# Kernel optimization log

Measured on AMD Instinct MI355X. Metric: run time of the kernel, lower is better.

The kernel has to match this reference:

```python
import jax, jax.numpy as jnp
import numpy as np

N_NODES = 50000
NEG_SLOPE = 0.2  # PyG GATConv default LeakyReLU slope


def gat_conv(x, src, dst, W, att_src, att_dst, bias, heads, out_ch, concat):
    """PyG-style GATConv (dropout=0, add_self_loops omitted to match raw edge list usage).
    x: [N, in], W: [in, heads*out_ch], att_*: [1, heads, out_ch], bias: [heads*out_ch] or [out_ch].
    Messages flow src -> dst; softmax normalizes over incoming edges of each dst node."""
    N = x.shape[0]
    h = (x @ W).reshape(N, heads, out_ch)                      # [N,H,C]
    a_s = (h * att_src).sum(-1)                                # [N,H]
    a_d = (h * att_dst).sum(-1)                                # [N,H]
    e = jax.nn.leaky_relu(a_s[src] + a_d[dst], NEG_SLOPE)      # [E,H] per-edge logits
    m = jax.ops.segment_max(e, dst, num_segments=N)            # [N,H] stable softmax max
    p = jnp.exp(e - m[dst])                                    # [E,H]
    s = jax.ops.segment_sum(p, dst, num_segments=N)            # [N,H]
    alpha = p / (s[dst] + 1e-16)                               # [E,H] attention coeffs
    out = jax.ops.segment_sum(h[src] * alpha[:, :, None], dst, num_segments=N)  # [N,H,C]
    out = out.reshape(N, heads * out_ch) if concat else out.mean(axis=1)
    return out + bias


def setup_inputs() -> dict:
    key = jax.random.key(0)
    ks = jax.random.split(key, 10)
    in_ch, hid, heads, out_ch = 128, 32, 4, 64
    E = 800000
    x = jax.random.normal(ks[0], (N_NODES, in_ch), dtype=jnp.float32)
    edge_index = jax.random.randint(ks[1], (2, E), 0, N_NODES, dtype=jnp.int64)
    sc = 0.1
    return {
        "x": x,
        "edge_index": edge_index,
        "W1": jax.random.normal(ks[2], (in_ch, heads * hid), dtype=jnp.float32) * sc,
        "att_src1": jax.random.normal(ks[3], (1, heads, hid), dtype=jnp.float32) * sc,
        "att_dst1": jax.random.normal(ks[4], (1, heads, hid), dtype=jnp.float32) * sc,
        "b1": jnp.zeros((heads * hid,), dtype=jnp.float32),
        "W2": jax.random.normal(ks[5], (heads * hid, out_ch), dtype=jnp.float32) * sc,
        "att_src2": jax.random.normal(ks[6], (1, 1, out_ch), dtype=jnp.float32) * sc,
        "att_dst2": jax.random.normal(ks[7], (1, 1, out_ch), dtype=jnp.float32) * sc,
        "b2": jnp.zeros((out_ch,), dtype=jnp.float32),
    }


def reference(x, edge_index, W1, att_src1, att_dst1, b1, W2, att_src2, att_dst2, b2):
    src, dst = edge_index[0], edge_index[1]
    h = gat_conv(x, src, dst, W1, att_src1, att_dst1, b1, heads=4, out_ch=32, concat=True)
    h = jax.nn.elu(h)
    out = gat_conv(h, src, dst, W2, att_src2, att_dst2, b2, heads=1, out_ch=64, concat=False)
    return out
```

## Files before the change

kernel.cpp:

```cpp
#include <hip/hip_runtime.h>

#define N_NODES 50000
#define N_EDGES 800000
#define GEMM_BLKS ((N_NODES + 63) / 64)
#define FILL_BLKS 4096
#define RANGE 6250
#define EDGES_PER_BLK 1564
#define MAXDEG 64
#define AGG_BLKS (N_NODES / 4)
#define W1P_ITEMS (144 * 136)
#define W2P_ITEMS (80 * 136)

typedef __attribute__((ext_vector_type(8))) short bf16x8;
typedef __attribute__((ext_vector_type(4))) float f32x4;
typedef unsigned short u16;
typedef unsigned int u32;

__device__ __forceinline__ float lrelu(float x) { return x > 0.f ? x : 0.2f * x; }

__device__ __forceinline__ u16 f2bf(float f) {
    u32 u = __float_as_uint(f);
    return (u16)((u + 0x7FFFu + ((u >> 16) & 1u)) >> 16);
}
__device__ __forceinline__ float bflo(u32 w) { return __uint_as_float(w << 16); }
__device__ __forceinline__ float bfhi(u32 w) { return __uint_as_float(w & 0xFFFF0000u); }
__device__ __forceinline__ float elu(float x) { return x > 0.f ? x : __expf(x) - 1.f; }

__global__ __launch_bounds__(256) void k_prep(
    const float* __restrict__ W1, const float* __restrict__ as1v, const float* __restrict__ ad1v,
    const float* __restrict__ W2, const float* __restrict__ as2v, const float* __restrict__ ad2v,
    u16* __restrict__ Wt1p, u16* __restrict__ Wt2p, int* __restrict__ deg)
{
    int gid = blockIdx.x * 256 + threadIdx.x;
    for (int i = gid; i < N_NODES; i += 120 * 256) deg[i] = 0;
    if (gid < W1P_ITEMS) {
        int n = gid / 136, k = gid % 136;
        float v = 0.f;
        if (k < 128) {
            if (n < 128) v = W1[k * 128 + n];
            else if (n < 136) {
                int h = n - 128;
                const float* att = (h < 4) ? as1v : ad1v;
                int hh = h & 3;
                float s = 0.f;
                for (int c = 0; c < 32; ++c) s += W1[k * 128 + hh * 32 + c] * att[hh * 32 + c];
                v = s;
            }
        }
        Wt1p[gid] = f2bf(v);
    } else {
        int g2 = gid - W1P_ITEMS;
        if (g2 < W2P_ITEMS) {
            int n = g2 / 136, k = g2 % 136;
            float v = 0.f;
            if (k < 128) {
                if (n < 64) v = W2[k * 64 + n];
                else if (n == 64) { float s = 0.f; for (int c = 0; c < 64; ++c) s += W2[k * 64 + c] * as2v[c]; v = s; }
                else if (n == 65) { float s = 0.f; for (int c = 0; c < 64; ++c) s += W2[k * 64 + c] * ad2v[c]; v = s; }
            }
            Wt2p[g2] = f2bf(v);
        }
    }
}

__global__ __launch_bounds__(256) void k_fill(
    const int* __restrict__ src, const int* __restrict__ dst,
    int* __restrict__ deg, u16* __restrict__ col16)
{
    const int g = blockIdx.x & 7;
    const int b = blockIdx.x >> 3;
    const int lo = g * RANGE;
    const int hi = min(lo + RANGE, N_NODES);
    const int e0 = b * EDGES_PER_BLK;
    const int e1 = min(e0 + EDGES_PER_BLK, N_EDGES);
    for (int e = e0 + threadIdx.x; e < e1; e += 256) {
        int v = dst[e];
        if (v >= lo && v < hi) {
            int pos = atomicAdd(&deg[v], 1);
            if (pos < MAXDEG) col16[v * MAXDEG + pos] = (u16)src[e];
        }
    }
}

__global__ __launch_bounds__(256, 4) void k_gemm1(
    const float* __restrict__ x, const u16* __restrict__ Wt1p,
    u16* __restrict__ hbf, float* __restrict__ as_, float* __restrict__ ad_)
{
    __shared__ u16 ws[144][136];
    const int t = threadIdx.x;
    const int n0 = blockIdx.x * 64;
    const int l = t & 63, w = t >> 6;
    const int lm = l & 15, quad = l >> 4;
    #pragma unroll
    for (int it = 0; it < 10; ++it) {
        int idx = it * 256 + t;
        if (idx < 2448) ((uint4*)&ws[0][0])[idx] = ((const uint4*)Wt1p)[idx];
    }
    const int nrow = n0 + w * 16 + lm;
    bf16x8 af[4];
    if (nrow < N_NODES) {
        const float* xr = &x[(size_t)nrow * 128];
        #pragma unroll
        for (int kc = 0; kc < 4; ++kc) {
            int k0 = kc * 32 + quad * 8;
            float4 v0 = *(const float4*)&xr[k0];
            float4 v1 = *(const float4*)&xr[k0 + 4];
            bf16x8 a;
            a[0] = (short)f2bf(v0.x); a[1] = (short)f2bf(v0.y);
            a[2] = (short)f2bf(v0.z); a[3] = (short)f2bf(v0.w);
            a[4] = (short)f2bf(v1.x); a[5] = (short)f2bf(v1.y);
            a[6] = (short)f2bf(v1.z); a[7] = (short)f2bf(v1.w);
            af[kc] = a;
        }
    } else {
        #pragma unroll
        for (int kc = 0; kc < 4; ++kc) af[kc] = (bf16x8){0, 0, 0, 0, 0, 0, 0, 0};
    }
    __syncthreads();
    f32x4 acc[9];
    #pragma unroll
    for (int nt = 0; nt < 9; ++nt) acc[nt] = (f32x4){0.f, 0.f, 0.f, 0.f};
    #pragma unroll
    for (int kc = 0; kc < 4; ++kc) {
        int k0 = kc * 32 + quad * 8;
        #pragma unroll
        for (int nt = 0; nt < 9; ++nt) {
            bf16x8 b = *(const bf16x8*)&ws[nt * 16 + lm][k0];
            acc[nt] = __builtin_amdgcn_mfma_f32_16x16x32_bf16(af[kc], b, acc[nt], 0, 0, 0);
        }
    }
    #pragma unroll
    for (int r = 0; r < 4; ++r) {
        int n = n0 + w * 16 + quad * 4 + r;
        if (n >= N_NODES) continue;
        #pragma unroll
        for (int nt = 0; nt < 8; ++nt)
            hbf[(size_t)n * 128 + nt * 16 + lm] = f2bf(acc[nt][r]);
        if (lm < 4)      as_[n * 4 + lm]     = acc[8][r];
        else if (lm < 8) ad_[n * 4 + lm - 4] = acc[8][r];
    }
}

__global__ __launch_bounds__(256) void k_agg1(
    const int* __restrict__ deg, const u16* __restrict__ col16,
    const float* __restrict__ as_, const float* __restrict__ ad_,
    const u32* __restrict__ h1u, const float* __restrict__ b1,
    u32* __restrict__ out1u)
{
    const int t = threadIdx.x;
    const int wv = t >> 6;
    const int l = t & 63;
    const int v = blockIdx.x * 4 + wv;
    const int c = l & 15;
    const int slot = l >> 4;
    const int hh = c >> 2;
    const int dg = min(deg[v], MAXDEG);
    const float adh = ad_[v * 4 + hh];
    const u16* cr = col16 + v * MAXDEG;
    float a[8] = {0.f, 0.f, 0.f, 0.f, 0.f, 0.f, 0.f, 0.f};
    float s = 0.f;
    for (int i0 = slot; i0 < dg; i0 += 8) {
        int i1 = i0 + 4;
        bool m1 = i1 < dg;
        int u0 = cr[i0];
        int u1 = cr[m1 ? i1 : i0];
        float p0 = __expf(lrelu(as_[u0 * 4 + hh] + adh));
        float p1 = m1 ? __expf(lrelu(as_[u1 * 4 + hh] + adh)) : 0.f;
        uint4 w0 = *(const uint4*)(h1u + (u0 << 6) + (c << 2));
        uint4 w1 = *(const uint4*)(h1u + (u1 << 6) + (c << 2));
        a[0] = fmaf(p0, bflo(w0.x), a[0]); a[1] = fmaf(p0, bfhi(w0.x), a[1]);
        a[2] = fmaf(p0, bflo(w0.y), a[2]); a[3] = fmaf(p0, bfhi(w0.y), a[3]);
        a[4] = fmaf(p0, bflo(w0.z), a[4]); a[5] = fmaf(p0, bfhi(w0.z), a[5]);
        a[6] = fmaf(p0, bflo(w0.w), a[6]); a[7] = fmaf(p0, bfhi(w0.w), a[7]);
        a[0] = fmaf(p1, bflo(w1.x), a[0]); a[1] = fmaf(p1, bfhi(w1.x), a[1]);
        a[2] = fmaf(p1, bflo(w1.y), a[2]); a[3] = fmaf(p1, bfhi(w1.y), a[3]);
        a[4] = fmaf(p1, bflo(w1.z), a[4]); a[5] = fmaf(p1, bfhi(w1.z), a[5]);
        a[6] = fmaf(p1, bflo(w1.w), a[6]); a[7] = fmaf(p1, bfhi(w1.w), a[7]);
        s += p0 + p1;
    }
    #pragma unroll
    for (int k = 0; k < 8; ++k) {
        a[k] += __shfl_xor(a[k], 16);
        a[k] += __shfl_xor(a[k], 32);
    }
    s += __shfl_xor(s, 16);
    s += __shfl_xor(s, 32);
    if (slot == 0) {
        float inv = 1.f / (s + 1e-16f);
        float4 b0 = *(const float4*)&b1[8 * c];
        float4 b4 = *(const float4*)&b1[8 * c + 4];
        float o0 = elu(a[0] * inv + b0.x);
        float o1 = elu(a[1] * inv + b0.y);
        float o2 = elu(a[2] * inv + b0.z);
        float o3 = elu(a[3] * inv + b0.w);
        float o4 = elu(a[4] * inv + b4.x);
        float o5 = elu(a[5] * inv + b4.y);
        float o6 = elu(a[6] * inv + b4.z);
        float o7 = elu(a[7] * inv + b4.w);
        uint4 pk;
        pk.x = (u32)f2bf(o0) | ((u32)f2bf(o1) << 16);
        pk.y = (u32)f2bf(o2) | ((u32)f2bf(o3) << 16);
        pk.z = (u32)f2bf(o4) | ((u32)f2bf(o5) << 16);
        pk.w = (u32)f2bf(o6) | ((u32)f2bf(o7) << 16);
        *(uint4*)(out1u + v * 64 + 4 * c) = pk;
    }
}

__global__ __launch_bounds__(256, 6) void k_gemm2(
    const u16* __restrict__ xbf, const u16* __restrict__ Wt2p,
    u16* __restrict__ hbf, float* __restrict__ as_, float* __restrict__ ad_)
{
    __shared__ u16 ws[80][136];
    const int t = threadIdx.x;
    const int n0 = blockIdx.x * 64;
    const int l = t & 63, w = t >> 6;
    const int lm = l & 15, quad = l >> 4;
    #pragma unroll
    for (int it = 0; it < 6; ++it) {
        int idx = it * 256 + t;
        if (idx < 1360) ((uint4*)&ws[0][0])[idx] = ((const uint4*)Wt2p)[idx];
    }
    const int nrow = n0 + w * 16 + lm;
    bf16x8 af[4];
    if (nrow < N_NODES) {
        const u16* xr = &xbf[(size_t)nrow * 128];
        #pragma unroll
        for (int kc = 0; kc < 4; ++kc)
            af[kc] = *(const bf16x8*)&xr[kc * 32 + quad * 8];
    } else {
        #pragma unroll
        for (int kc = 0; kc < 4; ++kc) af[kc] = (bf16x8){0, 0, 0, 0, 0, 0, 0, 0};
    }
    __syncthreads();
    f32x4 acc[5];
    #pragma unroll
    for (int nt = 0; nt < 5; ++nt) acc[nt] = (f32x4){0.f, 0.f, 0.f, 0.f};
    #pragma unroll
    for (int kc = 0; kc < 4; ++kc) {
        int k0 = kc * 32 + quad * 8;
        #pragma unroll
        for (int nt = 0; nt < 5; ++nt) {
            bf16x8 b = *(const bf16x8*)&ws[nt * 16 + lm][k0];
            acc[nt] = __builtin_amdgcn_mfma_f32_16x16x32_bf16(af[kc], b, acc[nt], 0, 0, 0);
        }
    }
    #pragma unroll
    for (int r = 0; r < 4; ++r) {
        int n = n0 + w * 16 + quad * 4 + r;
        if (n >= N_NODES) continue;
        #pragma unroll
        for (int nt = 0; nt < 4; ++nt)
            hbf[(size_t)n * 64 + nt * 16 + lm] = f2bf(acc[nt][r]);
        if (lm == 0)      as_[n] = acc[4][r];
        else if (lm == 1) ad_[n] = acc[4][r];
    }
}

__global__ __launch_bounds__(256) void k_agg2(
    const int* __restrict__ deg, const u16* __restrict__ col16,
    const float* __restrict__ as_, const float* __restrict__ ad_,
    const u32* __restrict__ h2u, const float* __restrict__ b2,
    float* __restrict__ out)
{
    const int t = threadIdx.x;
    const int wv = t >> 6;
    const int l = t & 63;
    const int v = blockIdx.x * 4 + wv;
    const int c = l & 7;
    const int slot = l >> 3;
    const int dg = min(deg[v], MAXDEG);
    const float adh = ad_[v];
    const u16* cr = col16 + v * MAXDEG;
    float a[8] = {0.f, 0.f, 0.f, 0.f, 0.f, 0.f, 0.f, 0.f};
    float s = 0.f;
    for (int i0 = slot; i0 < dg; i0 += 16) {
        int i1 = i0 + 8;
        bool m1 = i1 < dg;
        int u0 = cr[i0];
        int u1 = cr[m1 ? i1 : i0];
        float p0 = __expf(lrelu(as_[u0] + adh));
        float p1 = m1 ? __expf(lrelu(as_[u1] + adh)) : 0.f;
        uint4 w0 = *(const uint4*)(h2u + (u0 << 5) + (c << 2));
        uint4 w1 = *(const uint4*)(h2u + (u1 << 5) + (c << 2));
        a[0] = fmaf(p0, bflo(w0.x), a[0]); a[1] = fmaf(p0, bfhi(w0.x), a[1]);
        a[2] = fmaf(p0, bflo(w0.y), a[2]); a[3] = fmaf(p0, bfhi(w0.y), a[3]);
        a[4] = fmaf(p0, bflo(w0.z), a[4]); a[5] = fmaf(p0, bfhi(w0.z), a[5]);
        a[6] = fmaf(p0, bflo(w0.w), a[6]); a[7] = fmaf(p0, bfhi(w0.w), a[7]);
        a[0] = fmaf(p1, bflo(w1.x), a[0]); a[1] = fmaf(p1, bfhi(w1.x), a[1]);
        a[2] = fmaf(p1, bflo(w1.y), a[2]); a[3] = fmaf(p1, bfhi(w1.y), a[3]);
        a[4] = fmaf(p1, bflo(w1.z), a[4]); a[5] = fmaf(p1, bfhi(w1.z), a[5]);
        a[6] = fmaf(p1, bflo(w1.w), a[6]); a[7] = fmaf(p1, bfhi(w1.w), a[7]);
        s += p0 + p1;
    }
    #pragma unroll
    for (int k = 0; k < 8; ++k) {
        a[k] += __shfl_xor(a[k], 8);
        a[k] += __shfl_xor(a[k], 16);
        a[k] += __shfl_xor(a[k], 32);
    }
    s += __shfl_xor(s, 8);
    s += __shfl_xor(s, 16);
    s += __shfl_xor(s, 32);
    if (slot == 0) {
        float inv = 1.f / (s + 1e-16f);
        float4 b0 = *(const float4*)&b2[8 * c];
        float4 b4 = *(const float4*)&b2[8 * c + 4];
        float4 oa, ob;
        oa.x = a[0] * inv + b0.x;
        oa.y = a[1] * inv + b0.y;
        oa.z = a[2] * inv + b0.z;
        oa.w = a[3] * inv + b0.w;
        ob.x = a[4] * inv + b4.x;
        ob.y = a[5] * inv + b4.y;
        ob.z = a[6] * inv + b4.z;
        ob.w = a[7] * inv + b4.w;
        *(float4*)&out[(size_t)v * 64 + 8 * c]     = oa;
        *(float4*)&out[(size_t)v * 64 + 8 * c + 4] = ob;
    }
}

extern "C" void kernel_launch(void* const* d_in, const int* in_sizes, int n_in,
                              void* d_out, int out_size, void* d_ws, size_t ws_size,
                              hipStream_t stream)
{
    const float* x      = (const float*)d_in[0];
    const int*   ei     = (const int*)d_in[1];
    const float* W1     = (const float*)d_in[2];
    const float* att_s1 = (const float*)d_in[3];
    const float* att_d1 = (const float*)d_in[4];
    const float* b1     = (const float*)d_in[5];
    const float* W2     = (const float*)d_in[6];
    const float* att_s2 = (const float*)d_in[7];
    const float* att_d2 = (const float*)d_in[8];
    const float* b2     = (const float*)d_in[9];
    const int* src = ei;
    const int* dst = ei + N_EDGES;
    float* out = (float*)d_out;

    char* wsp = (char*)d_ws;
    u16* Wt1p  = (u16*)wsp;  wsp += W1P_ITEMS * 2;
    u16* Wt2p  = (u16*)wsp;  wsp += W2P_ITEMS * 2;
    u16* h1bf  = (u16*)wsp;  wsp += (size_t)N_NODES * 128 * 2;
    u16* o1bf  = (u16*)wsp;  wsp += (size_t)N_NODES * 128 * 2;
    u16* h2bf  = (u16*)wsp;  wsp += (size_t)N_NODES * 64 * 2;
    float* as1 = (float*)wsp; wsp += (size_t)N_NODES * 4 * 4;
    float* ad1 = (float*)wsp; wsp += (size_t)N_NODES * 4 * 4;
    float* as2 = (float*)wsp; wsp += (size_t)N_NODES * 4;
    float* ad2 = (float*)wsp; wsp += (size_t)N_NODES * 4;
    int* deg   = (int*)wsp;   wsp += (size_t)N_NODES * 4;
    u16* col16 = (u16*)wsp;  wsp += (size_t)N_NODES * MAXDEG * 2;

    k_prep<<<120, 256, 0, stream>>>(W1, att_s1, att_d1, W2, att_s2, att_d2, Wt1p, Wt2p, deg);
    k_fill<<<FILL_BLKS, 256, 0, stream>>>(src, dst, deg, col16);

    k_gemm1<<<GEMM_BLKS, 256, 0, stream>>>(x, Wt1p, h1bf, as1, ad1);
    k_agg1<<<AGG_BLKS, 256, 0, stream>>>(deg, col16, as1, ad1, (const u32*)h1bf, b1, (u32*)o1bf);

    k_gemm2<<<GEMM_BLKS, 256, 0, stream>>>(o1bf, Wt2p, h2bf, as2, ad2);
    k_agg2<<<AGG_BLKS, 256, 0, stream>>>(deg, col16, as2, ad2, (const u32*)h2bf, b2, out);
}
```

Before: 204.6 us.

## Fuse CSR fill into first GEMM launch and unroll aggregation loops four-wide

Merges the edge-bucketing fill kernel and the layer-1 GEMM into one launch: the first GEMM_BLKS blocks run the GEMM and the remaining blocks run the fill, so the two independent stages can overlap. The fill now uses 4 destination-range groups instead of 8, so each edge is scanned fewer times, at the cost of more atomic contention per group. Both aggregation kernels now process four neighbors per iteration instead of two, issuing more independent gathers before doing the math to raise memory-level parallelism. The fill blocks also carry the GEMM's shared-memory allocation and launch bounds, which may limit how many fill blocks run at once.

```diff
diff --git a/kernel.cpp b/kernel.cpp
--- a/kernel.cpp
+++ b/kernel.cpp
@@ -3,11 +3,13 @@
 #define N_NODES 50000
 #define N_EDGES 800000
 #define GEMM_BLKS ((N_NODES + 63) / 64)
-#define FILL_BLKS 4096
-#define RANGE 6250
+#define FILL_GROUPS 4
+#define FILL_BLKS (FILL_GROUPS * 512)
+#define RANGE 12500
 #define EDGES_PER_BLK 1564
 #define MAXDEG 64
 #define AGG_BLKS (N_NODES / 4)
+#define FG_BLKS (GEMM_BLKS + FILL_BLKS)
 #define W1P_ITEMS (144 * 136)
 #define W2P_ITEMS (80 * 136)
 
@@ -25,6 +27,13 @@
 __device__ __forceinline__ float bflo(u32 w) { return __uint_as_float(w << 16); }
 __device__ __forceinline__ float bfhi(u32 w) { return __uint_as_float(w & 0xFFFF0000u); }
 __device__ __forceinline__ float elu(float x) { return x > 0.f ? x : __expf(x) - 1.f; }
+
+#define FMA8(p_, w_) do { \
+    a[0] = fmaf(p_, bflo(w_.x), a[0]); a[1] = fmaf(p_, bfhi(w_.x), a[1]); \
+    a[2] = fmaf(p_, bflo(w_.y), a[2]); a[3] = fmaf(p_, bfhi(w_.y), a[3]); \
+    a[4] = fmaf(p_, bflo(w_.z), a[4]); a[5] = fmaf(p_, bfhi(w_.z), a[5]); \
+    a[6] = fmaf(p_, bflo(w_.w), a[6]); a[7] = fmaf(p_, bfhi(w_.w), a[7]); \
+} while (0)
 
 __global__ __launch_bounds__(256) void k_prep(
     const float* __restrict__ W1, const float* __restrict__ as1v, const float* __restrict__ ad1v,
@@ -63,31 +72,31 @@
     }
 }
 
-__global__ __launch_bounds__(256) void k_fill(
+__global__ __launch_bounds__(256, 4) void k_fg1(
+    const float* __restrict__ x, const u16* __restrict__ Wt1p,
+    u16* __restrict__ hbf, float* __restrict__ as_, float* __restrict__ ad_,
     const int* __restrict__ src, const int* __restrict__ dst,
     int* __restrict__ deg, u16* __restrict__ col16)
 {
-    const int g = blockIdx.x & 7;
-    const int b = blockIdx.x >> 3;
-    const int lo = g * RANGE;
-    const int hi = min(lo + RANGE, N_NODES);
-    const int e0 = b * EDGES_PER_BLK;
-    const int e1 = min(e0 + EDGES_PER_BLK, N_EDGES);
-    for (int e = e0 + threadIdx.x; e < e1; e += 256) {
-        int v = dst[e];
-        if (v >= lo && v < hi) {
-            int pos = atomicAdd(&deg[v], 1);
-            if (pos < MAXDEG) col16[v * MAXDEG + pos] = (u16)src[e];
-        }
-    }
-}
-
-__global__ __launch_bounds__(256, 4) void k_gemm1(
-    const float* __restrict__ x, const u16* __restrict__ Wt1p,
-    u16* __restrict__ hbf, float* __restrict__ as_, float* __restrict__ ad_)
-{
     __shared__ u16 ws[144][136];
     const int t = threadIdx.x;
+    if (blockIdx.x >= GEMM_BLKS) {
+        const int bb = blockIdx.x - GEMM_BLKS;
+        const int g = bb & (FILL_GROUPS - 1);
+        const int b = bb >> 2;
+        const int lo = g * RANGE;
+        const int hi = min(lo + RANGE, N_NODES);
+        const int e0 = b * EDGES_PER_BLK;
+        const int e1 = min(e0 + EDGES_PER_BLK, N_EDGES);
+        for (int e = e0 + t; e < e1; e += 256) {
+            int v = dst[e];
+            if (v >= lo && v < hi) {
+                int pos = atomicAdd(&deg[v], 1);
+                if (pos < MAXDEG) col16[v * MAXDEG + pos] = (u16)src[e];
+            }
+        }
+        return;
+    }
     const int n0 = blockIdx.x * 64;
     const int l = t & 63, w = t >> 6;
     const int lm = l & 15, quad = l >> 4;
@@ -159,24 +168,27 @@
     const u16* cr = col16 + v * MAXDEG;
     float a[8] = {0.f, 0.f, 0.f, 0.f, 0.f, 0.f, 0.f, 0.f};
     float s = 0.f;
-    for (int i0 = slot; i0 < dg; i0 += 8) {
-        int i1 = i0 + 4;
-        bool m1 = i1 < dg;
+    for (int i0 = slot; i0 < dg; i0 += 16) {
+        int j1 = i0 + 4, j2 = i0 + 8, j3 = i0 + 12;
+        bool m1 = j1 < dg, m2 = j2 < dg, m3 = j3 < dg;
         int u0 = cr[i0];
-        int u1 = cr[m1 ? i1 : i0];
-        float p0 = __expf(lrelu(as_[u0 * 4 + hh] + adh));
-        float p1 = m1 ? __expf(lrelu(as_[u1 * 4 + hh] + adh)) : 0.f;
+        int u1 = cr[m1 ? j1 : i0];
+        int u2 = cr[m2 ? j2 : i0];
+        int u3 = cr[m3 ? j3 : i0];
+        float e0 = as_[u0 * 4 + hh];
+        float e1 = as_[u1 * 4 + hh];
+        float e2 = as_[u2 * 4 + hh];
+        float e3 = as_[u3 * 4 + hh];
         uint4 w0 = *(const uint4*)(h1u + (u0 << 6) + (c << 2));
         uint4 w1 = *(const uint4*)(h1u + (u1 << 6) + (c << 2));
-        a[0] = fmaf(p0, bflo(w0.x), a[0]); a[1] = fmaf(p0, bfhi(w0.x), a[1]);
-        a[2] = fmaf(p0, bflo(w0.y), a[2]); a[3] = fmaf(p0, bfhi(w0.y), a[3]);
-        a[4] = fmaf(p0, bflo(w0.z), a[4]); a[5] = fmaf(p0, bfhi(w0.z), a[5]);
-        a[6] = fmaf(p0, bflo(w0.w), a[6]); a[7] = fmaf(p0, bfhi(w0.w), a[7]);
-        a[0] = fmaf(p1, bflo(w1.x), a[0]); a[1] = fmaf(p1, bfhi(w1.x), a[1]);
-        a[2] = fmaf(p1, bflo(w1.y), a[2]); a[3] = fmaf(p1, bfhi(w1.y), a[3]);
-        a[4] = fmaf(p1, bflo(w1.z), a[4]); a[5] = fmaf(p1, bfhi(w1.z), a[5]);
-        a[6] = fmaf(p1, bflo(w1.w), a[6]); a[7] = fmaf(p1, bfhi(w1.w), a[7]);
-        s += p0 + p1;
+        uint4 w2 = *(const uint4*)(h1u + (u2 << 6) + (c << 2));
+        uint4 w3 = *(const uint4*)(h1u + (u3 << 6) + (c << 2));
+        float p0 = __expf(lrelu(e0 + adh));
+        float p1 = m1 ? __expf(lrelu(e1 + adh)) : 0.f;
+        float p2 = m2 ? __expf(lrelu(e2 + adh)) : 0.f;
+        float p3 = m3 ? __expf(lrelu(e3 + adh)) : 0.f;
+        FMA8(p0, w0); FMA8(p1, w1); FMA8(p2, w2); FMA8(p3, w3);
+        s += (p0 + p1) + (p2 + p3);
     }
     #pragma unroll
     for (int k = 0; k < 8; ++k) {
@@ -273,24 +285,27 @@
     const u16* cr = col16 + v * MAXDEG;
     float a[8] = {0.f, 0.f, 0.f, 0.f, 0.f, 0.f, 0.f, 0.f};
     float s = 0.f;
-    for (int i0 = slot; i0 < dg; i0 += 16) {
-        int i1 = i0 + 8;
-        bool m1 = i1 < dg;
+    for (int i0 = slot; i0 < dg; i0 += 32) {
+        int j1 = i0 + 8, j2 = i0 + 16, j3 = i0 + 24;
+        bool m1 = j1 < dg, m2 = j2 < dg, m3 = j3 < dg;
         int u0 = cr[i0];
-        int u1 = cr[m1 ? i1 : i0];
-        float p0 = __expf(lrelu(as_[u0] + adh));
-        float p1 = m1 ? __expf(lrelu(as_[u1] + adh)) : 0.f;
+        int u1 = cr[m1 ? j1 : i0];
+        int u2 = cr[m2 ? j2 : i0];
+        int u3 = cr[m3 ? j3 : i0];
+        float e0 = as_[u0];
+        float e1 = as_[u1];
+        float e2 = as_[u2];
+        float e3 = as_[u3];
         uint4 w0 = *(const uint4*)(h2u + (u0 << 5) + (c << 2));
         uint4 w1 = *(const uint4*)(h2u + (u1 << 5) + (c << 2));
-        a[0] = fmaf(p0, bflo(w0.x), a[0]); a[1] = fmaf(p0, bfhi(w0.x), a[1]);
-        a[2] = fmaf(p0, bflo(w0.y), a[2]); a[3] = fmaf(p0, bfhi(w0.y), a[3]);
-        a[4] = fmaf(p0, bflo(w0.z), a[4]); a[5] = fmaf(p0, bfhi(w0.z), a[5]);
-        a[6] = fmaf(p0, bflo(w0.w), a[6]); a[7] = fmaf(p0, bfhi(w0.w), a[7]);
-        a[0] = fmaf(p1, bflo(w1.x), a[0]); a[1] = fmaf(p1, bfhi(w1.x), a[1]);
-        a[2] = fmaf(p1, bflo(w1.y), a[2]); a[3] = fmaf(p1, bfhi(w1.y), a[3]);
-        a[4] = fmaf(p1, bflo(w1.z), a[4]); a[5] = fmaf(p1, bfhi(w1.z), a[5]);
-        a[6] = fmaf(p1, bflo(w1.w), a[6]); a[7] = fmaf(p1, bfhi(w1.w), a[7]);
-        s += p0 + p1;
+        uint4 w2 = *(const uint4*)(h2u + (u2 << 5) + (c << 2));
+        uint4 w3 = *(const uint4*)(h2u + (u3 << 5) + (c << 2));
+        float p0 = __expf(lrelu(e0 + adh));
+        float p1 = m1 ? __expf(lrelu(e1 + adh)) : 0.f;
+        float p2 = m2 ? __expf(lrelu(e2 + adh)) : 0.f;
+        float p3 = m3 ? __expf(lrelu(e3 + adh)) : 0.f;
+        FMA8(p0, w0); FMA8(p1, w1); FMA8(p2, w2); FMA8(p3, w3);
+        s += (p0 + p1) + (p2 + p3);
     }
     #pragma unroll
     for (int k = 0; k < 8; ++k) {
@@ -351,9 +366,9 @@
     u16* col16 = (u16*)wsp;  wsp += (size_t)N_NODES * MAXDEG * 2;
 
     k_prep<<<120, 256, 0, stream>>>(W1, att_s1, att_d1, W2, att_s2, att_d2, Wt1p, Wt2p, deg);
-    k_fill<<<FILL_BLKS, 256, 0, stream>>>(src, dst, deg, col16);
-
-    k_gemm1<<<GEMM_BLKS, 256, 0, stream>>>(x, Wt1p, h1bf, as1, ad1);
+
+    k_fg1<<<FG_BLKS, 256, 0, stream>>>(x, Wt1p, h1bf, as1, ad1, src, dst, deg, col16);
+
     k_agg1<<<AGG_BLKS, 256, 0, stream>>>(deg, col16, as1, ad1, (const u32*)h1bf, b1, (u32*)o1bf);
 
     k_gemm2<<<GEMM_BLKS, 256, 0, stream>>>(o1bf, Wt2p, h2bf, as2, ad2);
```

Result: faster. 191.0 us (-6.6%).
